# Kernel optimization log

Hardware: AMD Instinct MI355X
Metric: run time of the kernel (lower is better)

The kernel has to match this reference:

```python
import jax, jax.numpy as jnp
import numpy as np

TEMPERATURE = 1.0
ITERATIONS = 5


def setup_inputs() -> dict:
    key = jax.random.key(0)
    logits = jax.random.normal(key, (64, 1024, 1024), dtype=jnp.float32)
    return {"logits": logits}


def reference(logits) -> jnp.ndarray:
    # Sinkhorn-Knopp in log space: alternate row and column log-normalization.
    def body(log_alpha, _):
        log_alpha = log_alpha - jax.nn.logsumexp(log_alpha, axis=2, keepdims=True)
        log_alpha = log_alpha - jax.nn.logsumexp(log_alpha, axis=1, keepdims=True)
        return log_alpha, None

    log_alpha, _ = jax.lax.scan(body, logits, None, length=ITERATIONS)
    return jnp.exp(log_alpha / TEMPERATURE)
```

## Files before the change

### kernel.cpp

```cpp
#include <hip/hip_runtime.h>


constexpr int BATCH = 64;
constexpr int N = 1024;
constexpr int ROWS_PER_WAVE = 16;
constexpr int WAVES_PER_WG = 4;
constexpr int PASS_BLOCKS = (BATCH * N) / (ROWS_PER_WAVE * WAVES_PER_WG);
constexpr int NSLOT = PASS_BLOCKS / BATCH;
constexpr int FINAL_BLOCKS = 16384;

template <bool PASS1>
__global__ __launch_bounds__(256) void sinkhorn_pass_kernel(
    const float* __restrict__ logits, const float* __restrict__ rcprev,
    float* __restrict__ u, float* __restrict__ partials) {
    __shared__ float lds[WAVES_PER_WG * N];

    const int tid = threadIdx.x;
    const int lane = tid & 63;
    const int wid = tid >> 6;
    const int wave_g = blockIdx.x * WAVES_PER_WG + wid;
    const int row0 = wave_g * ROWS_PER_WAVE;
    const int b = row0 >> 10;

    float4 rc[4];
    if constexpr (!PASS1) {
        const float4* cb = reinterpret_cast<const float4*>(rcprev + (b << 10));
#pragma unroll
        for (int c = 0; c < 4; ++c) rc[c] = cb[c * 64 + lane];
    }

    float4 acc[4];
#pragma unroll
    for (int c = 0; c < 4; ++c) acc[c] = make_float4(0.f, 0.f, 0.f, 0.f);

    const float4* lb =
        reinterpret_cast<const float4*>(logits) + (size_t)row0 * (N / 4) + lane;

    auto LOADR = [&](float4* X, int r) {
#pragma unroll
        for (int c = 0; c < 4; ++c) X[c] = lb[r * (N / 4) + c * 64];
    };

    auto PROCESS = [&](float4* X, int r) {
        float4 sv = make_float4(0.f, 0.f, 0.f, 0.f);
#pragma unroll
        for (int c = 0; c < 4; ++c) {
            X[c].x = __expf(X[c].x);
            X[c].y = __expf(X[c].y);
            X[c].z = __expf(X[c].z);
            X[c].w = __expf(X[c].w);
            if constexpr (PASS1) {
                sv.x += X[c].x;
                sv.y += X[c].y;
                sv.z += X[c].z;
                sv.w += X[c].w;
            } else {
                sv.x = fmaf(X[c].x, rc[c].x, sv.x);
                sv.y = fmaf(X[c].y, rc[c].y, sv.y);
                sv.z = fmaf(X[c].z, rc[c].z, sv.z);
                sv.w = fmaf(X[c].w, rc[c].w, sv.w);
            }
        }
        float s = (sv.x + sv.y) + (sv.z + sv.w);
#pragma unroll
        for (int off = 32; off >= 1; off >>= 1) s += __shfl_xor(s, off);
        if (lane == 0) u[row0 + r] = __logf(s);
        const float rinv = __builtin_amdgcn_rcpf(s);
#pragma unroll
        for (int c = 0; c < 4; ++c) {
            acc[c].x = fmaf(X[c].x, rinv, acc[c].x);
            acc[c].y = fmaf(X[c].y, rinv, acc[c].y);
            acc[c].z = fmaf(X[c].z, rinv, acc[c].z);
            acc[c].w = fmaf(X[c].w, rinv, acc[c].w);
        }
    };

    float4 A[4], B[4], C[4], D[4];
    LOADR(A, 0);
    LOADR(B, 1);
    LOADR(C, 2);
#pragma unroll
    for (int r = 0; r < ROWS_PER_WAVE; r += 4) {
        LOADR(D, r + 3);
        PROCESS(A, r);
        if (r + 4 < ROWS_PER_WAVE) LOADR(A, r + 4);
        PROCESS(B, r + 1);
        if (r + 5 < ROWS_PER_WAVE) LOADR(B, r + 5);
        PROCESS(C, r + 2);
        if (r + 6 < ROWS_PER_WAVE) LOADR(C, r + 6);
        PROCESS(D, r + 3);
    }

    float4* lw = reinterpret_cast<float4*>(lds + wid * N);
#pragma unroll
    for (int c = 0; c < 4; ++c) lw[c * 64 + lane] = acc[c];
    __syncthreads();

    const int j0 = tid * 4;
    float4 s0 = *reinterpret_cast<const float4*>(lds + 0 * N + j0);
    const float4 s1 = *reinterpret_cast<const float4*>(lds + 1 * N + j0);
    const float4 s2 = *reinterpret_cast<const float4*>(lds + 2 * N + j0);
    const float4 s3 = *reinterpret_cast<const float4*>(lds + 3 * N + j0);
    s0.x += s1.x + s2.x + s3.x;
    s0.y += s1.y + s2.y + s3.y;
    s0.z += s1.z + s2.z + s3.z;
    s0.w += s1.w + s2.w + s3.w;
    *reinterpret_cast<float4*>(partials + (size_t)blockIdx.x * N + j0) = s0;
}

template <bool LAST>
__global__ __launch_bounds__(256) void colred_kernel(const float* __restrict__ partials,
                                                     float* __restrict__ out) {
    const int t = blockIdx.x * 256 + threadIdx.x;
    const int e = t << 2;
    const int b = e >> 10;
    const int j = e & 1023;
    const float4* p =
        reinterpret_cast<const float4*>(partials + (size_t)(b * NSLOT) * N + j);
    float4 s = make_float4(0.f, 0.f, 0.f, 0.f);
#pragma unroll
    for (int k = 0; k < NSLOT; ++k) {
        const float4 x = p[k * (N / 4)];
        s.x += x.x;
        s.y += x.y;
        s.z += x.z;
        s.w += x.w;
    }
    float4 o;
    if constexpr (LAST) {
        o.x = __logf(s.x);
        o.y = __logf(s.y);
        o.z = __logf(s.z);
        o.w = __logf(s.w);
    } else {
        o.x = 1.0f / s.x;
        o.y = 1.0f / s.y;
        o.z = 1.0f / s.z;
        o.w = 1.0f / s.w;
    }
    *reinterpret_cast<float4*>(out + e) = o;
}

__global__ __launch_bounds__(256) void final_kernel(const float* __restrict__ logits,
                                                    const float* __restrict__ u,
                                                    const float* __restrict__ v,
                                                    float* __restrict__ out) {
    const int g0 = blockIdx.x * 256 + threadIdx.x;
#pragma unroll
    for (int p = 0; p < 4; ++p) {
        const int g = g0 + p * (FINAL_BLOCKS * 256);
        const int e = g << 2;
        const int r = e >> 10;
        const int jc = e & 1023;
        const int b = r >> 10;
        const float ur = u[r];
        const float4 vv = *reinterpret_cast<const float4*>(v + (b << 10) + jc);
        const float4 x = *reinterpret_cast<const float4*>(logits + (size_t)e);
        float4 o;
        o.x = __expf(x.x - ur - vv.x);
        o.y = __expf(x.y - ur - vv.y);
        o.z = __expf(x.z - ur - vv.z);
        o.w = __expf(x.w - ur - vv.w);
        *reinterpret_cast<float4*>(out + (size_t)e) = o;
    }
}

extern "C" void kernel_launch(void* const* d_in, const int* in_sizes, int n_in,
                              void* d_out, int out_size, void* d_ws, size_t ws_size,
                              hipStream_t stream) {
    const float* logits = (const float*)d_in[0];
    float* out = (float*)d_out;
    float* ws = (float*)d_ws;
    float* u = ws;
    float* v = ws + 65536;
    float* rc = ws + 2 * 65536;
    float* partials = out;

    sinkhorn_pass_kernel<true><<<PASS_BLOCKS, 256, 0, stream>>>(logits, rc, u, partials);
    colred_kernel<false><<<64, 256, 0, stream>>>(partials, rc);
    for (int it = 1; it < 4; ++it) {
        sinkhorn_pass_kernel<false><<<PASS_BLOCKS, 256, 0, stream>>>(logits, rc, u,
                                                                     partials);
        colred_kernel<false><<<64, 256, 0, stream>>>(partials, rc);
    }
    sinkhorn_pass_kernel<false><<<PASS_BLOCKS, 256, 0, stream>>>(logits, rc, u,
                                                                 partials);
    colred_kernel<true><<<64, 256, 0, stream>>>(partials, v);
    final_kernel<<<FINAL_BLOCKS, 256, 0, stream>>>(logits, u, v, out);
}
```

Before: 685.4 us.

## Cache exp(logits) in fp16 and fuse column reduction into next pass

```diff
diff --git a/kernel.cpp b/kernel.cpp
--- a/kernel.cpp
+++ b/kernel.cpp
@@ -1,70 +1,61 @@
 #include <hip/hip_runtime.h>
-
-
-constexpr int BATCH = 64;
+#include <hip/hip_fp16.h>
+
+
 constexpr int N = 1024;
+constexpr int NQ = N / 4;
 constexpr int ROWS_PER_WAVE = 16;
 constexpr int WAVES_PER_WG = 4;
-constexpr int PASS_BLOCKS = (BATCH * N) / (ROWS_PER_WAVE * WAVES_PER_WG);
-constexpr int NSLOT = PASS_BLOCKS / BATCH;
+constexpr int PASS_BLOCKS = (64 * N) / (ROWS_PER_WAVE * WAVES_PER_WG);
+constexpr int NSLOT = PASS_BLOCKS / 64;
 constexpr int FINAL_BLOCKS = 16384;
 
-template <bool PASS1>
-__global__ __launch_bounds__(256) void sinkhorn_pass_kernel(
-    const float* __restrict__ logits, const float* __restrict__ rcprev,
-    float* __restrict__ u, float* __restrict__ partials) {
-    __shared__ float lds[WAVES_PER_WG * N];
-
+using f4 = __attribute__((ext_vector_type(4))) float;
+
+struct H4 {
+    __half2 lo, hi;
+};
+
+__global__ __launch_bounds__(256) __attribute__((amdgpu_waves_per_eu(4, 4))) void
+pass1_kernel(const float* __restrict__ logits, __half* __restrict__ t,
+             float* __restrict__ pout) {
+    __shared__ float lacc[WAVES_PER_WG * N];
     const int tid = threadIdx.x;
     const int lane = tid & 63;
     const int wid = tid >> 6;
-    const int wave_g = blockIdx.x * WAVES_PER_WG + wid;
-    const int row0 = wave_g * ROWS_PER_WAVE;
-    const int b = row0 >> 10;
-
-    float4 rc[4];
-    if constexpr (!PASS1) {
-        const float4* cb = reinterpret_cast<const float4*>(rcprev + (b << 10));
-#pragma unroll
-        for (int c = 0; c < 4; ++c) rc[c] = cb[c * 64 + lane];
-    }
+    const int row0 = (blockIdx.x * WAVES_PER_WG + wid) * ROWS_PER_WAVE;
 
     float4 acc[4];
 #pragma unroll
     for (int c = 0; c < 4; ++c) acc[c] = make_float4(0.f, 0.f, 0.f, 0.f);
 
-    const float4* lb =
-        reinterpret_cast<const float4*>(logits) + (size_t)row0 * (N / 4) + lane;
-
-    auto LOADR = [&](float4* X, int r) {
-#pragma unroll
-        for (int c = 0; c < 4; ++c) X[c] = lb[r * (N / 4) + c * 64];
-    };
-
-    auto PROCESS = [&](float4* X, int r) {
+    const f4* lb = reinterpret_cast<const f4*>(logits) + (size_t)row0 * NQ + lane;
+    H4* tb = reinterpret_cast<H4*>(t) + (size_t)row0 * NQ + lane;
+
+    auto LOADR = [&](f4* X, int r) {
+#pragma unroll
+        for (int c = 0; c < 4; ++c)
+            X[c] = __builtin_nontemporal_load(lb + r * NQ + c * 64);
+    };
+    auto PROCESS = [&](f4* X, int r) {
         float4 sv = make_float4(0.f, 0.f, 0.f, 0.f);
 #pragma unroll
         for (int c = 0; c < 4; ++c) {
-            X[c].x = __expf(X[c].x);
-            X[c].y = __expf(X[c].y);
-            X[c].z = __expf(X[c].z);
-            X[c].w = __expf(X[c].w);
-            if constexpr (PASS1) {
-                sv.x += X[c].x;
-                sv.y += X[c].y;
-                sv.z += X[c].z;
-                sv.w += X[c].w;
-            } else {
-                sv.x = fmaf(X[c].x, rc[c].x, sv.x);
-                sv.y = fmaf(X[c].y, rc[c].y, sv.y);
-                sv.z = fmaf(X[c].z, rc[c].z, sv.z);
-                sv.w = fmaf(X[c].w, rc[c].w, sv.w);
-            }
+            X[c].x = __expf(X[c].x); sv.x += X[c].x;
+            X[c].y = __expf(X[c].y); sv.y += X[c].y;
+            X[c].z = __expf(X[c].z); sv.z += X[c].z;
+            X[c].w = __expf(X[c].w); sv.w += X[c].w;
+        }
+#pragma unroll
+        for (int c = 0; c < 4; ++c) {
+            H4 h;
+            h.lo = __floats2half2_rn(X[c].x, X[c].y);
+            h.hi = __floats2half2_rn(X[c].z, X[c].w);
+            tb[r * NQ + c * 64] = h;
         }
         float s = (sv.x + sv.y) + (sv.z + sv.w);
 #pragma unroll
         for (int off = 32; off >= 1; off >>= 1) s += __shfl_xor(s, off);
-        if (lane == 0) u[row0 + r] = __logf(s);
         const float rinv = __builtin_amdgcn_rcpf(s);
 #pragma unroll
         for (int c = 0; c < 4; ++c) {
@@ -75,10 +66,8 @@
         }
     };
 
-    float4 A[4], B[4], C[4], D[4];
-    LOADR(A, 0);
-    LOADR(B, 1);
-    LOADR(C, 2);
+    f4 A[4], B[4], C[4], D[4];
+    LOADR(A, 0); LOADR(B, 1); LOADR(C, 2);
 #pragma unroll
     for (int r = 0; r < ROWS_PER_WAVE; r += 4) {
         LOADR(D, r + 3);
@@ -91,60 +80,148 @@
         PROCESS(D, r + 3);
     }
 
-    float4* lw = reinterpret_cast<float4*>(lds + wid * N);
+    float4* lw = reinterpret_cast<float4*>(lacc + wid * N);
 #pragma unroll
     for (int c = 0; c < 4; ++c) lw[c * 64 + lane] = acc[c];
     __syncthreads();
-
     const int j0 = tid * 4;
-    float4 s0 = *reinterpret_cast<const float4*>(lds + 0 * N + j0);
-    const float4 s1 = *reinterpret_cast<const float4*>(lds + 1 * N + j0);
-    const float4 s2 = *reinterpret_cast<const float4*>(lds + 2 * N + j0);
-    const float4 s3 = *reinterpret_cast<const float4*>(lds + 3 * N + j0);
+    float4 s0 = *reinterpret_cast<const float4*>(lacc + 0 * N + j0);
+    const float4 s1 = *reinterpret_cast<const float4*>(lacc + 1 * N + j0);
+    const float4 s2 = *reinterpret_cast<const float4*>(lacc + 2 * N + j0);
+    const float4 s3 = *reinterpret_cast<const float4*>(lacc + 3 * N + j0);
     s0.x += s1.x + s2.x + s3.x;
     s0.y += s1.y + s2.y + s3.y;
     s0.z += s1.z + s2.z + s3.z;
     s0.w += s1.w + s2.w + s3.w;
-    *reinterpret_cast<float4*>(partials + (size_t)blockIdx.x * N + j0) = s0;
+    *reinterpret_cast<float4*>(pout + (size_t)blockIdx.x * N + j0) = s0;
 }
 
 template <bool LAST>
-__global__ __launch_bounds__(256) void colred_kernel(const float* __restrict__ partials,
-                                                     float* __restrict__ out) {
-    const int t = blockIdx.x * 256 + threadIdx.x;
-    const int e = t << 2;
+__global__ __launch_bounds__(256) __attribute__((amdgpu_waves_per_eu(4, 4))) void
+passk_kernel(const __half* __restrict__ t, const float* __restrict__ pin,
+             float* __restrict__ ri, float* __restrict__ pout) {
+    __shared__ float lacc[WAVES_PER_WG * N];
+    __shared__ float rcs[N];
+    const int tid = threadIdx.x;
+    const int lane = tid & 63;
+    const int wid = tid >> 6;
+    const int row0 = (blockIdx.x * WAVES_PER_WG + wid) * ROWS_PER_WAVE;
+    const int b = row0 >> 10;
+
+    const H4* tb = reinterpret_cast<const H4*>(t) + (size_t)row0 * NQ + lane;
+
+    auto LOADR = [&](H4* X, int r) {
+#pragma unroll
+        for (int c = 0; c < 4; ++c) X[c] = tb[r * NQ + c * 64];
+    };
+
+    H4 A[4], B[4], C[4], D[4];
+    LOADR(A, 0); LOADR(B, 1); LOADR(C, 2);
+
+    {
+        const float4* p4 =
+            reinterpret_cast<const float4*>(pin) + (size_t)(b * NSLOT) * NQ + tid;
+        float4 s4 = make_float4(0.f, 0.f, 0.f, 0.f);
+#pragma unroll
+        for (int k = 0; k < NSLOT; ++k) {
+            const float4 x = p4[k * NQ];
+            s4.x += x.x; s4.y += x.y; s4.z += x.z; s4.w += x.w;
+        }
+        float4 r4;
+        r4.x = 1.0f / s4.x; r4.y = 1.0f / s4.y;
+        r4.z = 1.0f / s4.z; r4.w = 1.0f / s4.w;
+        reinterpret_cast<float4*>(rcs)[tid] = r4;
+    }
+    __syncthreads();
+    float4 rc[4];
+#pragma unroll
+    for (int c = 0; c < 4; ++c) rc[c] = reinterpret_cast<const float4*>(rcs)[c * 64 + lane];
+
+    float4 acc[4];
+#pragma unroll
+    for (int c = 0; c < 4; ++c) acc[c] = make_float4(0.f, 0.f, 0.f, 0.f);
+
+    auto PROCESS = [&](H4* X, int r) {
+        float4 tf[4];
+        float4 sv = make_float4(0.f, 0.f, 0.f, 0.f);
+#pragma unroll
+        for (int c = 0; c < 4; ++c) {
+            const float2 l = __half22float2(X[c].lo);
+            const float2 h = __half22float2(X[c].hi);
+            tf[c] = make_float4(l.x, l.y, h.x, h.y);
+            sv.x = fmaf(tf[c].x, rc[c].x, sv.x);
+            sv.y = fmaf(tf[c].y, rc[c].y, sv.y);
+            sv.z = fmaf(tf[c].z, rc[c].z, sv.z);
+            sv.w = fmaf(tf[c].w, rc[c].w, sv.w);
+        }
+        float s = (sv.x + sv.y) + (sv.z + sv.w);
+#pragma unroll
+        for (int off = 32; off >= 1; off >>= 1) s += __shfl_xor(s, off);
+        const float rinv = __builtin_amdgcn_rcpf(s);
+        if constexpr (LAST) {
+            if (lane == 0) ri[row0 + r] = rinv;
+        }
+#pragma unroll
+        for (int c = 0; c < 4; ++c) {
+            acc[c].x = fmaf(tf[c].x, rinv, acc[c].x);
+            acc[c].y = fmaf(tf[c].y, rinv, acc[c].y);
+            acc[c].z = fmaf(tf[c].z, rinv, acc[c].z);
+            acc[c].w = fmaf(tf[c].w, rinv, acc[c].w);
+        }
+    };
+
+#pragma unroll
+    for (int r = 0; r < ROWS_PER_WAVE; r += 4) {
+        LOADR(D, r + 3);
+        PROCESS(A, r);
+        if (r + 4 < ROWS_PER_WAVE) LOADR(A, r + 4);
+        PROCESS(B, r + 1);
+        if (r + 5 < ROWS_PER_WAVE) LOADR(B, r + 5);
+        PROCESS(C, r + 2);
+        if (r + 6 < ROWS_PER_WAVE) LOADR(C, r + 6);
+        PROCESS(D, r + 3);
+    }
+
+    float4* lw = reinterpret_cast<float4*>(lacc + wid * N);
+#pragma unroll
+    for (int c = 0; c < 4; ++c) lw[c * 64 + lane] = acc[c];
+    __syncthreads();
+    const int j0 = tid * 4;
+    float4 s0 = *reinterpret_cast<const float4*>(lacc + 0 * N + j0);
+    const float4 s1 = *reinterpret_cast<const float4*>(lacc + 1 * N + j0);
+    const float4 s2 = *reinterpret_cast<const float4*>(lacc + 2 * N + j0);
+    const float4 s3 = *reinterpret_cast<const float4*>(lacc + 3 * N + j0);
+    s0.x += s1.x + s2.x + s3.x;
+    s0.y += s1.y + s2.y + s3.y;
+    s0.z += s1.z + s2.z + s3.z;
+    s0.w += s1.w + s2.w + s3.w;
+    *reinterpret_cast<float4*>(pout + (size_t)blockIdx.x * N + j0) = s0;
+}
+
+__global__ __launch_bounds__(256) void colred_kernel(const float* __restrict__ pin,
+                                                     float* __restrict__ rc5) {
+    const int tt = blockIdx.x * 256 + threadIdx.x;
+    const int e = tt << 2;
     const int b = e >> 10;
     const int j = e & 1023;
     const float4* p =
-        reinterpret_cast<const float4*>(partials + (size_t)(b * NSLOT) * N + j);
+        reinterpret_cast<const float4*>(pin) + (size_t)(b * NSLOT) * NQ + (j >> 2);
     float4 s = make_float4(0.f, 0.f, 0.f, 0.f);
 #pragma unroll
     for (int k = 0; k < NSLOT; ++k) {
-        const float4 x = p[k * (N / 4)];
-        s.x += x.x;
-        s.y += x.y;
-        s.z += x.z;
-        s.w += x.w;
+        const float4 x = p[k * NQ];
+        s.x += x.x; s.y += x.y; s.z += x.z; s.w += x.w;
     }
     float4 o;
-    if constexpr (LAST) {
-        o.x = __logf(s.x);
-        o.y = __logf(s.y);
-        o.z = __logf(s.z);
-        o.w = __logf(s.w);
-    } else {
-        o.x = 1.0f / s.x;
-        o.y = 1.0f / s.y;
-        o.z = 1.0f / s.z;
-        o.w = 1.0f / s.w;
-    }
-    *reinterpret_cast<float4*>(out + e) = o;
-}
-
-__global__ __launch_bounds__(256) void final_kernel(const float* __restrict__ logits,
-                                                    const float* __restrict__ u,
-                                                    const float* __restrict__ v,
-                                                    float* __restrict__ out) {
+    o.x = 1.0f / s.x; o.y = 1.0f / s.y; o.z = 1.0f / s.z; o.w = 1.0f / s.w;
+    *reinterpret_cast<float4*>(rc5 + e) = o;
+}
+
+template <bool USE_T>
+__global__ __launch_bounds__(256) void final_kernel(
+    const float* __restrict__ logits, const __half* __restrict__ t,
+    const float* __restrict__ ri, const float* __restrict__ rc5,
+    float* __restrict__ out) {
     const int g0 = blockIdx.x * 256 + threadIdx.x;
 #pragma unroll
     for (int p = 0; p < 4; ++p) {
@@ -153,15 +230,26 @@
         const int r = e >> 10;
         const int jc = e & 1023;
         const int b = r >> 10;
-        const float ur = u[r];
-        const float4 vv = *reinterpret_cast<const float4*>(v + (b << 10) + jc);
-        const float4 x = *reinterpret_cast<const float4*>(logits + (size_t)e);
-        float4 o;
-        o.x = __expf(x.x - ur - vv.x);
-        o.y = __expf(x.y - ur - vv.y);
-        o.z = __expf(x.z - ur - vv.z);
-        o.w = __expf(x.w - ur - vv.w);
-        *reinterpret_cast<float4*>(out + (size_t)e) = o;
+        const float rr = ri[r];
+        const float4 rv = *reinterpret_cast<const float4*>(rc5 + (b << 10) + jc);
+        f4 o;
+        if constexpr (USE_T) {
+            const H4 th = reinterpret_cast<const H4*>(t)[(size_t)r * NQ + (jc >> 2)];
+            const float2 l = __half22float2(th.lo);
+            const float2 h = __half22float2(th.hi);
+            o.x = l.x * rr * rv.x;
+            o.y = l.y * rr * rv.y;
+            o.z = h.x * rr * rv.z;
+            o.w = h.y * rr * rv.w;
+        } else {
+            const f4 x = __builtin_nontemporal_load(
+                reinterpret_cast<const f4*>(logits) + g);
+            o.x = __expf(x.x) * rr * rv.x;
+            o.y = __expf(x.y) * rr * rv.y;
+            o.z = __expf(x.z) * rr * rv.z;
+            o.w = __expf(x.w) * rr * rv.w;
+        }
+        __builtin_nontemporal_store(o, reinterpret_cast<f4*>(out) + g);
     }
 }
 
@@ -171,20 +259,23 @@
     const float* logits = (const float*)d_in[0];
     float* out = (float*)d_out;
     float* ws = (float*)d_ws;
-    float* u = ws;
-    float* v = ws + 65536;
-    float* rc = ws + 2 * 65536;
-    float* partials = out;
-
-    sinkhorn_pass_kernel<true><<<PASS_BLOCKS, 256, 0, stream>>>(logits, rc, u, partials);
-    colred_kernel<false><<<64, 256, 0, stream>>>(partials, rc);
-    for (int it = 1; it < 4; ++it) {
-        sinkhorn_pass_kernel<false><<<PASS_BLOCKS, 256, 0, stream>>>(logits, rc, u,
-                                                                     partials);
-        colred_kernel<false><<<64, 256, 0, stream>>>(partials, rc);
-    }
-    sinkhorn_pass_kernel<false><<<PASS_BLOCKS, 256, 0, stream>>>(logits, rc, u,
-                                                                 partials);
-    colred_kernel<true><<<64, 256, 0, stream>>>(partials, v);
-    final_kernel<<<FINAL_BLOCKS, 256, 0, stream>>>(logits, u, v, out);
-}
+    float* ri = ws;
+    float* rc5 = ws + 65536;
+    float* p0 = out;
+    float* p1 = out + (1 << 20);
+    const bool t_in_ws = ws_size >= (size_t)512 * 1024 + (size_t)128 * 1024 * 1024;
+    __half* t = t_in_ws ? reinterpret_cast<__half*>(ws + 2 * 65536)
+                        : reinterpret_cast<__half*>(out + (1 << 25));
+
+    pass1_kernel<<<PASS_BLOCKS, 256, 0, stream>>>(logits, t, p0);
+    passk_kernel<false><<<PASS_BLOCKS, 256, 0, stream>>>(t, p0, ri, p1);
+    passk_kernel<false><<<PASS_BLOCKS, 256, 0, stream>>>(t, p1, ri, p0);
+    passk_kernel<false><<<PASS_BLOCKS, 256, 0, stream>>>(t, p0, ri, p1);
+    passk_kernel<true><<<PASS_BLOCKS, 256, 0, stream>>>(t, p1, ri, p0);
+    colred_kernel<<<64, 256, 0, stream>>>(p0, rc5);
+    if (t_in_ws) {
+        final_kernel<true><<<FINAL_BLOCKS, 256, 0, stream>>>(logits, t, ri, rc5, out);
+    } else {
+        final_kernel<false><<<FINAL_BLOCKS, 256, 0, stream>>>(logits, t, ri, rc5, out);
+    }
+}
```

New measurement: 1.147 ms. +67.3%, slower.
